# Optimization experiments

Measured on AMD Instinct MI355X. Metric: run time of the kernel, lower is better.

## Reference

```python
import jax, jax.numpy as jnp
import numpy as np
from jax import lax

H = 1024  # hidden_dim

def _lstm_layer(x, h0, c0, W_ih, W_hh, b_ih, b_hh):
    # x: [B,T,I]; PyTorch gate order: i, f, g, o along the 4H axis.
    xg = jnp.einsum('bti,gi->btg', x, W_ih) + b_ih  # [B,T,4H], input projection precomputed

    def step(carry, xg_t):
        h, c = carry
        gates = xg_t + h @ W_hh.T + b_hh  # [B,4H]
        i, f, g, o = jnp.split(gates, 4, axis=-1)
        i = jax.nn.sigmoid(i)
        f = jax.nn.sigmoid(f)
        g = jnp.tanh(g)
        o = jax.nn.sigmoid(o)
        c = f * c + i * g
        h = o * jnp.tanh(c)
        return (h, c), h

    (_, _), hs = lax.scan(step, (h0, c0), jnp.swapaxes(xg, 0, 1))  # scan over T
    return jnp.swapaxes(hs, 0, 1)  # [B,T,H]


def setup_inputs() -> dict:
    key = jax.random.key(0)
    ks = jax.random.split(key, 13)
    B, T, I = 64, 512, 128
    s = 0.05
    return {
        'x': jax.random.normal(ks[0], (B, T, I), jnp.float32),
        'h0': jax.random.normal(ks[1], (2, B, H), jnp.float32),
        'c0': jax.random.normal(ks[2], (2, B, H), jnp.float32),
        'W_ih0': jax.random.normal(ks[3], (4 * H, I), jnp.float32) * s,
        'W_hh0': jax.random.normal(ks[4], (4 * H, H), jnp.float32) * s,
        'b_ih0': jax.random.normal(ks[5], (4 * H,), jnp.float32) * s,
        'b_hh0': jax.random.normal(ks[6], (4 * H,), jnp.float32) * s,
        'W_ih1': jax.random.normal(ks[7], (4 * H, H), jnp.float32) * s,
        'W_hh1': jax.random.normal(ks[8], (4 * H, H), jnp.float32) * s,
        'b_ih1': jax.random.normal(ks[9], (4 * H,), jnp.float32) * s,
        'b_hh1': jax.random.normal(ks[10], (4 * H,), jnp.float32) * s,
        'W_fc': jax.random.normal(ks[11], (1, H), jnp.float32) * s,
        'b_fc': jax.random.normal(ks[12], (1,), jnp.float32) * s,
    }


def reference(x, h0, c0, W_ih0, W_hh0, b_ih0, b_hh0, W_ih1, W_hh1, b_ih1, b_hh1, W_fc, b_fc):
    h1 = _lstm_layer(x, h0[0], c0[0], W_ih0, W_hh0, b_ih0, b_hh0)   # layer 0
    h2 = _lstm_layer(h1, h0[1], c0[1], W_ih1, W_hh1, b_ih1, b_hh1)  # layer 1
    out = jnp.einsum('bth,oh->bto', h2, W_fc) + b_fc                 # [B,T,1]
    return jnp.squeeze(out, axis=-1)                                 # [B,T]
```

## Files before the change

kernel.cpp:

```cpp
#include <hip/hip_runtime.h>

#define TT 512
#define II 128
#define HH 1024
#define BB 64

typedef __attribute__((ext_vector_type(8))) short bf16x8;
typedef __attribute__((ext_vector_type(4))) float f32x4;

__device__ __forceinline__ unsigned short f2bf(float f) {
  unsigned u = __builtin_bit_cast(unsigned, f);
  u += 0x7fffu + ((u >> 16) & 1u);
  return (unsigned short)(u >> 16);
}

__device__ __forceinline__ bf16x8 load8f_bf(const float* p) {
  const f32x4* q = (const f32x4*)p;
  f32x4 a = q[0];
  f32x4 b = q[1];
  bf16x8 r;
  r[0] = (short)f2bf(a[0]); r[1] = (short)f2bf(a[1]);
  r[2] = (short)f2bf(a[2]); r[3] = (short)f2bf(a[3]);
  r[4] = (short)f2bf(b[0]); r[5] = (short)f2bf(b[1]);
  r[6] = (short)f2bf(b[2]); r[7] = (short)f2bf(b[3]);
  return r;
}

__device__ __forceinline__ float sigm(float v) { return 1.f / (1.f + __expf(-v)); }
__device__ __forceinline__ float tanh_f(float v) { return 2.f / (1.f + __expf(-2.f * v)) - 1.f; }

__device__ __forceinline__ bf16x8 ld_h8(const unsigned short* p) {
  unsigned long long lo = __hip_atomic_load((unsigned long long*)p,
      __ATOMIC_RELAXED, __HIP_MEMORY_SCOPE_AGENT);
  unsigned long long hi = __hip_atomic_load((unsigned long long*)(p + 4),
      __ATOMIC_RELAXED, __HIP_MEMORY_SCOPE_AGENT);
  union { unsigned long long q[2]; bf16x8 v; } u;
  u.q[0] = lo; u.q[1] = hi;
  return u.v;
}

__device__ __forceinline__ void group_barrier(int* bar, int g, int rank, int tgt8) {
  __syncthreads();
  if (threadIdx.x < 64) {
    const int lane = threadIdx.x;
    if (lane == (rank & 7)) {
      __hip_atomic_fetch_add(bar + (g * 8 + lane) * 16, 1,
          __ATOMIC_RELAXED, __HIP_MEMORY_SCOPE_AGENT);
    }
    bool ok;
    do {
      int v = tgt8;
      if (lane < 8)
        v = __hip_atomic_load(bar + (g * 8 + lane) * 16,
            __ATOMIC_RELAXED, __HIP_MEMORY_SCOPE_AGENT);
      ok = __all(v >= tgt8);
      if (!ok) __builtin_amdgcn_s_sleep(1);
    } while (!ok);
  }
  __syncthreads();
}

__global__ __attribute__((amdgpu_flat_work_group_size(512, 512), amdgpu_waves_per_eu(2, 2)))
void lstm_persistent(
    const float* __restrict__ x, const float* __restrict__ h0,
    const float* __restrict__ c0,
    const float* __restrict__ Wih0, const float* __restrict__ Whh0,
    const float* __restrict__ bih0, const float* __restrict__ bhh0,
    const float* __restrict__ Wih1, const float* __restrict__ Whh1,
    const float* __restrict__ bih1, const float* __restrict__ bhh1,
    const float* __restrict__ Wfc, const float* __restrict__ bfc,
    float* __restrict__ out, unsigned short* __restrict__ hbuf, int* __restrict__ bar)
{
  const int tid  = threadIdx.x;
  const int lane = tid & 63;
  const int wv   = tid >> 6;
  const int L    = wv >> 2;
  const int kwv  = wv & 3;
  const int bid  = blockIdx.x;
  const int g    = bid >> 6;
  const int rank = bid & 63;
  const int gbase = g * 16;
  const int ubase = rank * 16;

  unsigned short* h1s = hbuf;
  unsigned short* h2s = hbuf + 2 * BB * HH;

  __shared__ float lds_part[2][4][64][17];
  __shared__ float lds_bias[128];
  __shared__ float lds_out[16];
  extern __shared__ __align__(16) unsigned short lds_w[];

  const int n  = lane & 15;
  const int ko = (lane >> 4) * 8;

  bf16x8 w[4][9];
  if (L == 0) {
#pragma unroll
    for (int nt = 0; nt < 4; ++nt) {
      int r = nt * 16 + n;
      int R = (r & 3) * HH + ubase + (r >> 2);
#pragma unroll
      for (int kt = 0; kt < 9; ++kt) {
        int c = kwv * 288 + kt * 32 + ko;
        const float* src = (c < II) ? (Wih0 + (size_t)R * II + c)
                                    : (Whh0 + (size_t)R * HH + (c - II));
        w[nt][kt] = load8f_bf(src);
      }
    }
  } else {
#pragma unroll
    for (int nt = 0; nt < 4; ++nt) {
      int r = nt * 16 + n;
      int R = (r & 3) * HH + ubase + (r >> 2);
#pragma unroll
      for (int kt = 0; kt < 16; ++kt) {
        int c = kwv * 512 + kt * 32 + ko;
        const float* src = (c < HH) ? (Wih1 + (size_t)R * HH + c)
                                    : (Whh1 + (size_t)R * HH + (c - HH));
        bf16x8 f = load8f_bf(src);
        if (kt < 9) {
          w[nt][kt] = f;
        } else {
          int fi = ((kwv * 7 + (kt - 9)) * 4 + nt) * 64 + lane;
          ((bf16x8*)lds_w)[fi] = f;
        }
      }
    }
  }

  if (tid < 128) {
    int Lr = tid >> 6, r = tid & 63;
    int R = (r & 3) * HH + ubase + (r >> 2);
    lds_bias[tid] = (Lr == 0) ? (bih0[R] + bhh0[R]) : (bih1[R] + bhh1[R]);
  }

  const int eL = tid >> 8;
  const int eu = tid & 15;
  const int em = (tid >> 4) & 15;
  const int b_e = gbase + em;
  const int u_e = ubase + eu;
  float c_st = c0[eL * BB * HH + b_e * HH + u_e];
  const float wfc_r = Wfc[u_e];

  if (rank < 16) {
    int b = gbase + rank;
    int u = tid * 2;
    unsigned p1 = (unsigned)f2bf(h0[0 * BB * HH + b * HH + u]) |
                  ((unsigned)f2bf(h0[0 * BB * HH + b * HH + u + 1]) << 16);
    unsigned p2 = (unsigned)f2bf(h0[1 * BB * HH + b * HH + u]) |
                  ((unsigned)f2bf(h0[1 * BB * HH + b * HH + u + 1]) << 16);
    __hip_atomic_store((unsigned*)(h1s + BB * HH + b * HH + u), p1,
        __ATOMIC_RELAXED, __HIP_MEMORY_SCOPE_AGENT);
    __hip_atomic_store((unsigned*)(h2s + BB * HH + b * HH + u), p2,
        __ATOMIC_RELAXED, __HIP_MEMORY_SCOPE_AGENT);
  }
  if (rank == 0) {
    float bf = bfc[0];
    for (int i = tid; i < 16 * TT; i += 512)
      __hip_atomic_store(&out[(gbase + (i >> 9)) * TT + (i & 511)], bf,
          __ATOMIC_RELAXED, __HIP_MEMORY_SCOPE_AGENT);
  }

  group_barrier(bar, g, rank, 8);

  const int bA = gbase + n;

  for (int p = 0; p <= TT; ++p) {
    const bool l0act = (p < TT);
    const bool l1act = (p >= 1);
    const unsigned short* h1r = h1s + ((p - 1) & 1) * (BB * HH);
    const unsigned short* h2r = h2s + (p & 1) * (BB * HH);

    f32x4 acc[4];
#pragma unroll
    for (int nt = 0; nt < 4; ++nt) acc[nt] = (f32x4){0.f, 0.f, 0.f, 0.f};

    if (L == 0) {
      if (l0act) {
        if (kwv == 0) {
#pragma unroll
          for (int kt = 0; kt < 4; ++kt) {
            bf16x8 a = load8f_bf(x + ((size_t)bA * TT + p) * II + kt * 32 + ko);
#pragma unroll
            for (int nt = 0; nt < 4; ++nt)
              acc[nt] = __builtin_amdgcn_mfma_f32_16x16x32_bf16(a, w[nt][kt], acc[nt], 0, 0, 0);
          }
#pragma unroll
          for (int kt = 4; kt < 9; ++kt) {
            bf16x8 a = ld_h8(h1r + (size_t)bA * HH + (kt * 32 + ko - II));
#pragma unroll
            for (int nt = 0; nt < 4; ++nt)
              acc[nt] = __builtin_amdgcn_mfma_f32_16x16x32_bf16(a, w[nt][kt], acc[nt], 0, 0, 0);
          }
        } else {
#pragma unroll
          for (int kt = 0; kt < 9; ++kt) {
            int off = kwv * 288 + kt * 32 + ko - II;
            bf16x8 a = ld_h8(h1r + (size_t)bA * HH + off);
#pragma unroll
            for (int nt = 0; nt < 4; ++nt)
              acc[nt] = __builtin_amdgcn_mfma_f32_16x16x32_bf16(a, w[nt][kt], acc[nt], 0, 0, 0);
          }
        }
      }
    } else {
      if (l1act) {
        const unsigned short* hb = (kwv < 2) ? h1r : h2r;
        const int kbase = (kwv & 1) * 512;
#pragma unroll
        for (int kt = 0; kt < 9; ++kt) {
          bf16x8 a = ld_h8(hb + (size_t)bA * HH + kbase + kt * 32 + ko);
#pragma unroll
          for (int nt = 0; nt < 4; ++nt)
            acc[nt] = __builtin_amdgcn_mfma_f32_16x16x32_bf16(a, w[nt][kt], acc[nt], 0, 0, 0);
        }
#pragma unroll
        for (int kt = 9; kt < 16; ++kt) {
          bf16x8 a = ld_h8(hb + (size_t)bA * HH + kbase + kt * 32 + ko);
#pragma unroll
          for (int nt = 0; nt < 4; ++nt) {
            bf16x8 wf = ((const bf16x8*)lds_w)[((kwv * 7 + (kt - 9)) * 4 + nt) * 64 + lane];
            acc[nt] = __builtin_amdgcn_mfma_f32_16x16x32_bf16(a, wf, acc[nt], 0, 0, 0);
          }
        }
      }
    }

    {
      const bool act = (L == 0) ? l0act : l1act;
      if (act) {
        const int m0 = (lane >> 4) * 4;
#pragma unroll
        for (int nt = 0; nt < 4; ++nt) {
          int row = nt * 16 + n;
#pragma unroll
          for (int r = 0; r < 4; ++r)
            lds_part[L][kwv][row][m0 + r] = acc[nt][r];
        }
      }
    }
    if (tid < 16) lds_out[tid] = 0.f;
    __syncthreads();

    const bool eact = (eL == 0) ? l0act : l1act;
    if (eact) {
      float pre[4];
#pragma unroll
      for (int q = 0; q < 4; ++q) {
        float s = lds_bias[eL * 64 + eu * 4 + q];
#pragma unroll
        for (int w2 = 0; w2 < 4; ++w2)
          s += lds_part[eL][w2][eu * 4 + q][em];
        pre[q] = s;
      }
      float iv = sigm(pre[0]);
      float fv = sigm(pre[1]);
      float gv = tanh_f(pre[2]);
      float ov = sigm(pre[3]);
      c_st = fv * c_st + iv * gv;
      float hv = ov * tanh_f(c_st);
      unsigned short hb16 = f2bf(hv);
      int partner = __shfl_xor((int)hb16, 1);
      unsigned short* hdst = (eL == 0) ? (h1s + (p & 1) * (BB * HH))
                                       : (h2s + ((p - 1) & 1) * (BB * HH));
      if ((lane & 1) == 0) {
        unsigned pk = (unsigned)hb16 | ((unsigned)partner << 16);
        __hip_atomic_store((unsigned*)(hdst + b_e * HH + u_e), pk,
            __ATOMIC_RELAXED, __HIP_MEMORY_SCOPE_AGENT);
      }
      if (eL == 1) atomicAdd(&lds_out[em], hv * wfc_r);
    }
    __syncthreads();
    if (l1act && tid < 16)
      atomicAdd(&out[(gbase + tid) * TT + (p - 1)], lds_out[tid]);

    if (p < TT) group_barrier(bar, g, rank, 8 * (p + 2));
  }
}

extern "C" void kernel_launch(void* const* d_in, const int* in_sizes, int n_in,
                              void* d_out, int out_size, void* d_ws, size_t ws_size,
                              hipStream_t stream) {
  (void)in_sizes; (void)n_in; (void)out_size; (void)ws_size;
  hipMemsetAsync(d_ws, 0, 4096, stream);
  int* bar = (int*)d_ws;
  unsigned short* hbuf = (unsigned short*)((char*)d_ws + 4096);
  hipLaunchKernelGGL(lstm_persistent, dim3(256), dim3(512), 114688, stream,
      (const float*)d_in[0], (const float*)d_in[1], (const float*)d_in[2],
      (const float*)d_in[3], (const float*)d_in[4], (const float*)d_in[5],
      (const float*)d_in[6], (const float*)d_in[7], (const float*)d_in[8],
      (const float*)d_in[9], (const float*)d_in[10], (const float*)d_in[11],
      (const float*)d_in[12], (float*)d_out, hbuf, bar);
}
```

Before: 4.541 ms.

## Retile LSTM blocks to 32 batches by 8 units and relax h-state memory ordering

Each workgroup now handles 32 batch rows and 8 hidden units instead of 16 by 16, so groups span 128 blocks and each wave issues 2x2 MFMA tiles that reuse every weight fragment across two batch tiles. More weights spill from registers into LDS, and the group barrier spreads its counters over 16 slots. Per-element atomic loads of h become plain vector loads, protected by an acquire fence after the barrier and by sc0/sc1 write-through stores plus an explicit vmcnt wait. The aim is to cut synchronisation and load overhead per step, at the cost of a barrier spanning twice as many blocks and more LDS weight traffic.

After: 6.091 ms. 34.1% more time.

```diff
diff --git a/kernel.cpp b/kernel.cpp
--- a/kernel.cpp
+++ b/kernel.cpp
@@ -29,38 +29,37 @@
 __device__ __forceinline__ float sigm(float v) { return 1.f / (1.f + __expf(-v)); }
 __device__ __forceinline__ float tanh_f(float v) { return 2.f / (1.f + __expf(-2.f * v)) - 1.f; }
 
-__device__ __forceinline__ bf16x8 ld_h8(const unsigned short* p) {
-  unsigned long long lo = __hip_atomic_load((unsigned long long*)p,
-      __ATOMIC_RELAXED, __HIP_MEMORY_SCOPE_AGENT);
-  unsigned long long hi = __hip_atomic_load((unsigned long long*)(p + 4),
-      __ATOMIC_RELAXED, __HIP_MEMORY_SCOPE_AGENT);
-  union { unsigned long long q[2]; bf16x8 v; } u;
-  u.q[0] = lo; u.q[1] = hi;
-  return u.v;
-}
-
-__device__ __forceinline__ void group_barrier(int* bar, int g, int rank, int tgt8) {
+__device__ __forceinline__ void st_short_sc(unsigned short* p, unsigned short v) {
+  unsigned vv = v;
+  asm volatile("global_store_short %0, %1, off sc0 sc1" :: "v"(p), "v"(vv) : "memory");
+}
+__device__ __forceinline__ void st_dword_sc(float* p, float v) {
+  asm volatile("global_store_dword %0, %1, off sc0 sc1" :: "v"(p), "v"(v) : "memory");
+}
+
+__device__ __forceinline__ void group_barrier(int* bar, int g, int rank, int tgt) {
   __syncthreads();
   if (threadIdx.x < 64) {
-    const int lane = threadIdx.x;
-    if (lane == (rank & 7)) {
-      __hip_atomic_fetch_add(bar + (g * 8 + lane) * 16, 1,
+    const int ln = threadIdx.x;
+    if (ln == (rank & 15)) {
+      __hip_atomic_fetch_add(bar + (g * 16 + ln) * 16, 1,
           __ATOMIC_RELAXED, __HIP_MEMORY_SCOPE_AGENT);
     }
     bool ok;
     do {
-      int v = tgt8;
-      if (lane < 8)
-        v = __hip_atomic_load(bar + (g * 8 + lane) * 16,
+      int v = tgt;
+      if (ln < 16)
+        v = __hip_atomic_load(bar + (g * 16 + ln) * 16,
             __ATOMIC_RELAXED, __HIP_MEMORY_SCOPE_AGENT);
-      ok = __all(v >= tgt8);
+      ok = __all(v >= tgt);
       if (!ok) __builtin_amdgcn_s_sleep(1);
     } while (!ok);
+    __builtin_amdgcn_fence(__ATOMIC_ACQUIRE, "agent");
   }
   __syncthreads();
 }
 
-__global__ __attribute__((amdgpu_flat_work_group_size(512, 512), amdgpu_waves_per_eu(2, 2)))
+__global__ __attribute__((amdgpu_waves_per_eu(2, 2))) __launch_bounds__(512)
 void lstm_persistent(
     const float* __restrict__ x, const float* __restrict__ h0,
     const float* __restrict__ c0,
@@ -77,26 +76,26 @@
   const int L    = wv >> 2;
   const int kwv  = wv & 3;
   const int bid  = blockIdx.x;
-  const int g    = bid >> 6;
-  const int rank = bid & 63;
-  const int gbase = g * 16;
-  const int ubase = rank * 16;
+  const int g    = bid >> 7;
+  const int rank = bid & 127;
+  const int gbase = g * 32;
+  const int ubase = rank * 8;
 
   unsigned short* h1s = hbuf;
   unsigned short* h2s = hbuf + 2 * BB * HH;
 
-  __shared__ float lds_part[2][4][64][17];
-  __shared__ float lds_bias[128];
-  __shared__ float lds_out[16];
+  __shared__ float lds_part[2][4][32][33];
+  __shared__ float lds_bias[64];
+  __shared__ float lds_out[32];
   extern __shared__ __align__(16) unsigned short lds_w[];
 
   const int n  = lane & 15;
   const int ko = (lane >> 4) * 8;
 
-  bf16x8 w[4][9];
+  bf16x8 w[2][6];
   if (L == 0) {
 #pragma unroll
-    for (int nt = 0; nt < 4; ++nt) {
+    for (int nt = 0; nt < 2; ++nt) {
       int r = nt * 16 + n;
       int R = (r & 3) * HH + ubase + (r >> 2);
 #pragma unroll
@@ -104,12 +103,17 @@
         int c = kwv * 288 + kt * 32 + ko;
         const float* src = (c < II) ? (Wih0 + (size_t)R * II + c)
                                     : (Whh0 + (size_t)R * HH + (c - II));
-        w[nt][kt] = load8f_bf(src);
+        bf16x8 f = load8f_bf(src);
+        if (kt < 5) {
+          w[nt][kt] = f;
+        } else {
+          ((bf16x8*)lds_w)[((kwv * 4 + (kt - 5)) * 2 + nt) * 64 + lane] = f;
+        }
       }
     }
   } else {
 #pragma unroll
-    for (int nt = 0; nt < 4; ++nt) {
+    for (int nt = 0; nt < 2; ++nt) {
       int r = nt * 16 + n;
       int R = (r & 3) * HH + ubase + (r >> 2);
 #pragma unroll
@@ -118,52 +122,50 @@
         const float* src = (c < HH) ? (Wih1 + (size_t)R * HH + c)
                                     : (Whh1 + (size_t)R * HH + (c - HH));
         bf16x8 f = load8f_bf(src);
-        if (kt < 9) {
+        if (kt < 6) {
           w[nt][kt] = f;
         } else {
-          int fi = ((kwv * 7 + (kt - 9)) * 4 + nt) * 64 + lane;
-          ((bf16x8*)lds_w)[fi] = f;
-        }
-      }
-    }
-  }
-
-  if (tid < 128) {
-    int Lr = tid >> 6, r = tid & 63;
+          ((bf16x8*)lds_w)[2048 + ((kwv * 10 + (kt - 6)) * 2 + nt) * 64 + lane] = f;
+        }
+      }
+    }
+  }
+
+  if (tid < 64) {
+    int Lr = tid >> 5, r = tid & 31;
     int R = (r & 3) * HH + ubase + (r >> 2);
     lds_bias[tid] = (Lr == 0) ? (bih0[R] + bhh0[R]) : (bih1[R] + bhh1[R]);
   }
 
   const int eL = tid >> 8;
-  const int eu = tid & 15;
-  const int em = (tid >> 4) & 15;
+  const int eu = tid & 7;
+  const int em = (tid >> 3) & 31;
   const int b_e = gbase + em;
   const int u_e = ubase + eu;
   float c_st = c0[eL * BB * HH + b_e * HH + u_e];
   const float wfc_r = Wfc[u_e];
 
-  if (rank < 16) {
+  if (rank < 32) {
     int b = gbase + rank;
     int u = tid * 2;
     unsigned p1 = (unsigned)f2bf(h0[0 * BB * HH + b * HH + u]) |
                   ((unsigned)f2bf(h0[0 * BB * HH + b * HH + u + 1]) << 16);
     unsigned p2 = (unsigned)f2bf(h0[1 * BB * HH + b * HH + u]) |
                   ((unsigned)f2bf(h0[1 * BB * HH + b * HH + u + 1]) << 16);
-    __hip_atomic_store((unsigned*)(h1s + BB * HH + b * HH + u), p1,
-        __ATOMIC_RELAXED, __HIP_MEMORY_SCOPE_AGENT);
-    __hip_atomic_store((unsigned*)(h2s + BB * HH + b * HH + u), p2,
-        __ATOMIC_RELAXED, __HIP_MEMORY_SCOPE_AGENT);
+    st_dword_sc((float*)(h1s + BB * HH + b * HH + u), __builtin_bit_cast(float, p1));
+    st_dword_sc((float*)(h2s + BB * HH + b * HH + u), __builtin_bit_cast(float, p2));
   }
   if (rank == 0) {
     float bf = bfc[0];
-    for (int i = tid; i < 16 * TT; i += 512)
-      __hip_atomic_store(&out[(gbase + (i >> 9)) * TT + (i & 511)], bf,
-          __ATOMIC_RELAXED, __HIP_MEMORY_SCOPE_AGENT);
-  }
-
-  group_barrier(bar, g, rank, 8);
-
-  const int bA = gbase + n;
+    for (int i = tid; i < 32 * TT; i += 512)
+      st_dword_sc(&out[(gbase + (i >> 9)) * TT + (i & 511)], bf);
+  }
+  asm volatile("s_waitcnt vmcnt(0)" ::: "memory");
+
+  group_barrier(bar, g, rank, 8 * 1);
+
+  const int bA0 = gbase + n;
+  const int bA1 = gbase + 16 + n;
 
   for (int p = 0; p <= TT; ++p) {
     const bool l0act = (p < TT);
@@ -171,35 +173,51 @@
     const unsigned short* h1r = h1s + ((p - 1) & 1) * (BB * HH);
     const unsigned short* h2r = h2s + (p & 1) * (BB * HH);
 
-    f32x4 acc[4];
-#pragma unroll
-    for (int nt = 0; nt < 4; ++nt) acc[nt] = (f32x4){0.f, 0.f, 0.f, 0.f};
+    f32x4 acc[2][2];
+#pragma unroll
+    for (int mt = 0; mt < 2; ++mt)
+#pragma unroll
+      for (int nt = 0; nt < 2; ++nt) acc[mt][nt] = (f32x4){0.f, 0.f, 0.f, 0.f};
 
     if (L == 0) {
       if (l0act) {
         if (kwv == 0) {
 #pragma unroll
           for (int kt = 0; kt < 4; ++kt) {
-            bf16x8 a = load8f_bf(x + ((size_t)bA * TT + p) * II + kt * 32 + ko);
-#pragma unroll
-            for (int nt = 0; nt < 4; ++nt)
-              acc[nt] = __builtin_amdgcn_mfma_f32_16x16x32_bf16(a, w[nt][kt], acc[nt], 0, 0, 0);
+            bf16x8 a0 = load8f_bf(x + ((size_t)bA0 * TT + p) * II + kt * 32 + ko);
+            bf16x8 a1 = load8f_bf(x + ((size_t)bA1 * TT + p) * II + kt * 32 + ko);
+#pragma unroll
+            for (int nt = 0; nt < 2; ++nt) {
+              acc[0][nt] = __builtin_amdgcn_mfma_f32_16x16x32_bf16(a0, w[nt][kt], acc[0][nt], 0, 0, 0);
+              acc[1][nt] = __builtin_amdgcn_mfma_f32_16x16x32_bf16(a1, w[nt][kt], acc[1][nt], 0, 0, 0);
+            }
           }
 #pragma unroll
           for (int kt = 4; kt < 9; ++kt) {
-            bf16x8 a = ld_h8(h1r + (size_t)bA * HH + (kt * 32 + ko - II));
-#pragma unroll
-            for (int nt = 0; nt < 4; ++nt)
-              acc[nt] = __builtin_amdgcn_mfma_f32_16x16x32_bf16(a, w[nt][kt], acc[nt], 0, 0, 0);
+            int off = kt * 32 + ko - II;
+            bf16x8 a0 = *(const bf16x8*)(h1r + (size_t)bA0 * HH + off);
+            bf16x8 a1 = *(const bf16x8*)(h1r + (size_t)bA1 * HH + off);
+#pragma unroll
+            for (int nt = 0; nt < 2; ++nt) {
+              bf16x8 wf = (kt < 5) ? w[nt][kt]
+                  : ((const bf16x8*)lds_w)[((kwv * 4 + (kt - 5)) * 2 + nt) * 64 + lane];
+              acc[0][nt] = __builtin_amdgcn_mfma_f32_16x16x32_bf16(a0, wf, acc[0][nt], 0, 0, 0);
+              acc[1][nt] = __builtin_amdgcn_mfma_f32_16x16x32_bf16(a1, wf, acc[1][nt], 0, 0, 0);
+            }
           }
         } else {
 #pragma unroll
           for (int kt = 0; kt < 9; ++kt) {
             int off = kwv * 288 + kt * 32 + ko - II;
-            bf16x8 a = ld_h8(h1r + (size_t)bA * HH + off);
-#pragma unroll
-            for (int nt = 0; nt < 4; ++nt)
-              acc[nt] = __builtin_amdgcn_mfma_f32_16x16x32_bf16(a, w[nt][kt], acc[nt], 0, 0, 0);
+            bf16x8 a0 = *(const bf16x8*)(h1r + (size_t)bA0 * HH + off);
+            bf16x8 a1 = *(const bf16x8*)(h1r + (size_t)bA1 * HH + off);
+#pragma unroll
+            for (int nt = 0; nt < 2; ++nt) {
+              bf16x8 wf = (kt < 5) ? w[nt][kt]
+                  : ((const bf16x8*)lds_w)[((kwv * 4 + (kt - 5)) * 2 + nt) * 64 + lane];
+              acc[0][nt] = __builtin_amdgcn_mfma_f32_16x16x32_bf16(a0, wf, acc[0][nt], 0, 0, 0);
+              acc[1][nt] = __builtin_amdgcn_mfma_f32_16x16x32_bf16(a1, wf, acc[1][nt], 0, 0, 0);
+            }
           }
         }
       }
@@ -208,19 +226,16 @@
         const unsigned short* hb = (kwv < 2) ? h1r : h2r;
         const int kbase = (kwv & 1) * 512;
 #pragma unroll
-        for (int kt = 0; kt < 9; ++kt) {
-          bf16x8 a = ld_h8(hb + (size_t)bA * HH + kbase + kt * 32 + ko);
-#pragma unroll
-          for (int nt = 0; nt < 4; ++nt)
-            acc[nt] = __builtin_amdgcn_mfma_f32_16x16x32_bf16(a, w[nt][kt], acc[nt], 0, 0, 0);
-        }
-#pragma unroll
-        for (int kt = 9; kt < 16; ++kt) {
-          bf16x8 a = ld_h8(hb + (size_t)bA * HH + kbase + kt * 32 + ko);
-#pragma unroll
-          for (int nt = 0; nt < 4; ++nt) {
-            bf16x8 wf = ((const bf16x8*)lds_w)[((kwv * 7 + (kt - 9)) * 4 + nt) * 64 + lane];
-            acc[nt] = __builtin_amdgcn_mfma_f32_16x16x32_bf16(a, wf, acc[nt], 0, 0, 0);
+        for (int kt = 0; kt < 16; ++kt) {
+          int off = kbase + kt * 32 + ko;
+          bf16x8 a0 = *(const bf16x8*)(hb + (size_t)bA0 * HH + off);
+          bf16x8 a1 = *(const bf16x8*)(hb + (size_t)bA1 * HH + off);
+#pragma unroll
+          for (int nt = 0; nt < 2; ++nt) {
+            bf16x8 wf = (kt < 6) ? w[nt][kt]
+                : ((const bf16x8*)lds_w)[2048 + ((kwv * 10 + (kt - 6)) * 2 + nt) * 64 + lane];
+            acc[0][nt] = __builtin_amdgcn_mfma_f32_16x16x32_bf16(a0, wf, acc[0][nt], 0, 0, 0);
+            acc[1][nt] = __builtin_amdgcn_mfma_f32_16x16x32_bf16(a1, wf, acc[1][nt], 0, 0, 0);
           }
         }
       }
@@ -231,15 +246,17 @@
       if (act) {
         const int m0 = (lane >> 4) * 4;
 #pragma unroll
-        for (int nt = 0; nt < 4; ++nt) {
+        for (int nt = 0; nt < 2; ++nt) {
           int row = nt * 16 + n;
 #pragma unroll
-          for (int r = 0; r < 4; ++r)
-            lds_part[L][kwv][row][m0 + r] = acc[nt][r];
-        }
-      }
-    }
-    if (tid < 16) lds_out[tid] = 0.f;
+          for (int mt = 0; mt < 2; ++mt)
+#pragma unroll
+            for (int r = 0; r < 4; ++r)
+              lds_part[L][kwv][row][mt * 16 + m0 + r] = acc[mt][nt][r];
+        }
+      }
+    }
+    if (tid < 32) lds_out[tid] = 0.f;
     __syncthreads();
 
     const bool eact = (eL == 0) ? l0act : l1act;
@@ -247,7 +264,7 @@
       float pre[4];
 #pragma unroll
       for (int q = 0; q < 4; ++q) {
-        float s = lds_bias[eL * 64 + eu * 4 + q];
+        float s = lds_bias[eL * 32 + eu * 4 + q];
 #pragma unroll
         for (int w2 = 0; w2 < 4; ++w2)
           s += lds_part[eL][w2][eu * 4 + q][em];
@@ -265,13 +282,13 @@
                                        : (h2s + ((p - 1) & 1) * (BB * HH));
       if ((lane & 1) == 0) {
         unsigned pk = (unsigned)hb16 | ((unsigned)partner << 16);
-        __hip_atomic_store((unsigned*)(hdst + b_e * HH + u_e), pk,
-            __ATOMIC_RELAXED, __HIP_MEMORY_SCOPE_AGENT);
+        st_dword_sc((float*)(hdst + b_e * HH + u_e), __builtin_bit_cast(float, pk));
       }
       if (eL == 1) atomicAdd(&lds_out[em], hv * wfc_r);
     }
+    asm volatile("s_waitcnt vmcnt(0)" ::: "memory");
     __syncthreads();
-    if (l1act && tid < 16)
+    if (l1act && tid < 32)
       atomicAdd(&out[(gbase + tid) * TT + (p - 1)], lds_out[tid]);
 
     if (p < TT) group_barrier(bar, g, rank, 8 * (p + 2));
```
